# Kernel tuning notes

Hardware: AMD Instinct MI355X
Metric: run time of the kernel (lower is better)

## Reference

```python
import jax, jax.numpy as jnp
import numpy as np

BETA = 0.25
NUM_EMBEDDINGS = 512
DIM_EMBEDDING = 64


def setup_inputs() -> dict:
    key = jax.random.key(0)
    k1, k2 = jax.random.split(key)
    z_e = jax.random.normal(k1, (32, 64, 64, 64), dtype=jnp.float32)
    # torch init: uniform_(-1/num_embeddings, 1/num_embeddings)
    lim = 1.0 / NUM_EMBEDDINGS
    embeddings = jax.random.uniform(
        k2, (NUM_EMBEDDINGS, DIM_EMBEDDING), dtype=jnp.float32,
        minval=-lim, maxval=lim)
    return {"z_e": z_e, "embeddings": embeddings}


def reference(z_e, embeddings):
    # Flatten exactly as torch's z_e.view(-1, dim_embedding) on (N,C,H,W)
    z_flat = z_e.reshape(-1, DIM_EMBEDDING)          # [M, D]
    # Squared euclidean distances: ||z||^2 + ||e||^2 - 2 z e^T
    distances = (
        jnp.sum(z_flat ** 2, axis=1, keepdims=True)
        + jnp.sum(embeddings ** 2, axis=1)
        - 2.0 * jnp.matmul(z_flat, embeddings.T)
    )                                                # [M, K]
    encoding_indices = jnp.argmin(distances, axis=1)[:, None]  # [M, 1]
    quantized = embeddings[encoding_indices[:, 0]].reshape(z_e.shape)
    # Straight-through estimator
    quantized_st = z_e + jax.lax.stop_gradient(quantized - z_e)
    recon_loss = jnp.mean((jax.lax.stop_gradient(quantized_st) - z_e) ** 2)
    commitment_loss = BETA * jnp.mean(
        (quantized_st - jax.lax.stop_gradient(z_e)) ** 2)
    loss = recon_loss + commitment_loss
    return (loss, quantized_st, encoding_indices)
```

## Files before the change

### kernel.cpp

```cpp
#include <hip/hip_runtime.h>
#include <hip/hip_bf16.h>

constexpr int NELEM = 8388608;
constexpr int ROWS  = 64;
constexpr int NBLK  = 131072 / ROWS;
constexpr int ZS    = 68;
constexpr float EPS = 1e-3f;
constexpr int QCAP  = 1024;

typedef short bf16x8 __attribute__((ext_vector_type(8)));
typedef float v4f    __attribute__((ext_vector_type(4)));

__device__ bf16x8 g_efrag[32][2][64];
__device__ float  g_en2[512];

__device__ inline bf16x8 cvt_hi8(const float* __restrict__ s, float scale) {
    bf16x8 h;
#pragma unroll
    for (int j = 0; j < 8; ++j) {
        __hip_bfloat16 b = __float2bfloat16(scale * s[j]);
        h[j] = (short)__bfloat16_as_ushort(b);
    }
    return h;
}

__global__ void __launch_bounds__(256) vq_prep(const float* __restrict__ emb,
                                               float* __restrict__ out) {
    const int b = blockIdx.x;
    if (b < 16) {
        const int id   = b * 256 + threadIdx.x;
        const int lane = id & 63;
        const int kc   = (id >> 6) & 1;
        const int ct   = id >> 7;
        const float* src = emb + (size_t)(ct * 16 + (lane & 15)) * 64
                               + kc * 32 + (lane >> 4) * 8;
        g_efrag[ct][kc][lane] = cvt_hi8(src, -2.0f);
    } else {
#pragma unroll
        for (int c = 0; c < 2; ++c) {
            const int k = threadIdx.x + c * 256;
            const float4* e4 = (const float4*)(emb + (size_t)k * 64);
            float a = 0.f, bq = 0.f, cc = 0.f, d = 0.f;
#pragma unroll
            for (int i = 0; i < 16; ++i) {
                float4 v = e4[i];
                a += v.x * v.x; bq += v.y * v.y; cc += v.z * v.z; d += v.w * v.w;
            }
            g_en2[k] = (a + bq) + (cc + d);
        }
        if (threadIdx.x == 0) out[0] = 0.f;
    }
}

__global__ __launch_bounds__(256) __attribute__((amdgpu_waves_per_eu(4, 4)))
void vq_main(const float* __restrict__ z,
             const float* __restrict__ emb,
             float* __restrict__ out) {
    __shared__ float s_z[ROWS * ZS];
    __shared__ float s_en2[512];
    __shared__ float s_zn2[ROWS];
    __shared__ unsigned long long s_key[ROWS];
    __shared__ unsigned s_q[QCAP];
    __shared__ int s_qn;
    __shared__ float s_lpart[4];

    const int tid  = threadIdx.x;
    const int lane = tid & 63;
    const int wid  = __builtin_amdgcn_readfirstlane(tid >> 6);
    const int mcol = lane & 15;
    const int quad = lane >> 4;

    {
        const int row = tid >> 2, seg = tid & 3;
        const float4* gp = (const float4*)(z + ((size_t)blockIdx.x * ROWS + row) * 64 + seg * 16);
#pragma unroll
        for (int i = 0; i < 4; ++i)
            *(float4*)&s_z[row * ZS + seg * 16 + i * 4] = gp[i];
    }
    s_en2[tid]       = g_en2[tid];
    s_en2[tid + 256] = g_en2[tid + 256];
    if (tid < ROWS) s_key[tid] = ~0ULL;
    if (tid == 0) s_qn = 0;
    __syncthreads();

    {
        const int row = tid >> 2, s = tid & 3;
        const float* zr = &s_z[row * ZS];
        float p = 0.f;
#pragma unroll
        for (int i = 0; i < 16; ++i) p += zr[4 * i + s] * zr[4 * i + s];
        p += __shfl_xor(p, 1, 64);
        p += __shfl_xor(p, 2, 64);
        if (s == 0) s_zn2[row] = p;
    }

    const int zrow = wid * 16 + mcol;
    const bf16x8 zf0 = cvt_hi8(&s_z[zrow * ZS +  0 + quad * 8], 1.0f);
    const bf16x8 zf1 = cvt_hi8(&s_z[zrow * ZS + 32 + quad * 8], 1.0f);

    float lmin = 3.402823466e38f;
#pragma unroll 4
    for (int ct = 0; ct < 32; ++ct) {
        bf16x8 e0 = g_efrag[ct][0][lane];
        bf16x8 e1 = g_efrag[ct][1][lane];
        v4f a = *(const v4f*)&s_en2[ct * 16 + quad * 4];
        a = __builtin_amdgcn_mfma_f32_16x16x32_bf16(e0, zf0, a, 0, 0, 0);
        a = __builtin_amdgcn_mfma_f32_16x16x32_bf16(e1, zf1, a, 0, 0, 0);
        lmin = fminf(lmin, fminf(fminf(a.x, a.y), fminf(a.z, a.w)));
    }
    lmin = fminf(lmin, __shfl_xor(lmin, 16, 64));
    lmin = fminf(lmin, __shfl_xor(lmin, 32, 64));
    const float thr = lmin + EPS;

#pragma unroll 4
    for (int ct = 0; ct < 32; ++ct) {
        bf16x8 e0 = g_efrag[ct][0][lane];
        bf16x8 e1 = g_efrag[ct][1][lane];
        v4f a = *(const v4f*)&s_en2[ct * 16 + quad * 4];
        a = __builtin_amdgcn_mfma_f32_16x16x32_bf16(e0, zf0, a, 0, 0, 0);
        a = __builtin_amdgcn_mfma_f32_16x16x32_bf16(e1, zf1, a, 0, 0, 0);
        float m4 = fminf(fminf(a.x, a.y), fminf(a.z, a.w));
        if (m4 <= thr) {
#pragma unroll
            for (int r = 0; r < 4; ++r) {
                if (a[r] <= thr) {
                    int slot = atomicAdd(&s_qn, 1);
                    if (slot < QCAP)
                        s_q[slot] = ((unsigned)zrow << 16) |
                                    (unsigned)(ct * 16 + quad * 4 + r);
                }
            }
        }
    }
    __syncthreads();

    {
        const int qn = s_qn;
        for (int i = tid; i < qn && i < QCAP; i += 256) {
            const unsigned e = s_q[i];
            const int row = e >> 16, code = e & 0xFFFF;
            const float* zr = &s_z[row * ZS];
            const float* er = emb + (size_t)code * 64;
            float a = 0.f, b = 0.f, c2 = 0.f, d = 0.f;
#pragma unroll
            for (int g = 0; g < 16; ++g) {
                a  += zr[4*g]   * er[4*g];   b += zr[4*g+1] * er[4*g+1];
                c2 += zr[4*g+2] * er[4*g+2]; d += zr[4*g+3] * er[4*g+3];
            }
            float dot  = (a + b) + (c2 + d);
            float dist = (s_zn2[row] + s_en2[code]) - 2.0f * dot;
            unsigned long long key =
                ((unsigned long long)__float_as_uint(dist) << 32) | (unsigned)code;
            atomicMin(&s_key[row], key);
        }
    }
    __syncthreads();

    const int row = tid >> 2, seg = tid & 3;
    const int widx = (int)(unsigned)(s_key[row] & 0x1FFULL);
    const float* er = emb + (size_t)widx * 64 + seg * 16;
    const float* zr = &s_z[row * ZS + seg * 16];
    float* qo = out + 1 + ((size_t)blockIdx.x * ROWS + row) * 64 + seg * 16;
    float lsum = 0.f;
#pragma unroll
    for (int j = 0; j < 16; ++j) {
        float zv = zr[j], ev = er[j];
        float q = zv + (ev - zv);
        float df = q - zv; lsum += df * df;
        qo[j] = q;
    }
    if (seg == 0)
        out[1 + NELEM + blockIdx.x * ROWS + row] = (float)widx;

#pragma unroll
    for (int off = 32; off; off >>= 1) lsum += __shfl_down(lsum, off, 64);
    if (lane == 0) s_lpart[wid] = lsum;
    __syncthreads();
    if (tid == 0) {
        float p = (s_lpart[0] + s_lpart[1]) + (s_lpart[2] + s_lpart[3]);
        atomicAdd(out, p * (1.25f / 8388608.0f));
    }
}

extern "C" void kernel_launch(void* const* d_in, const int* in_sizes, int n_in,
                              void* d_out, int out_size, void* d_ws, size_t ws_size,
                              hipStream_t stream) {
    const float* z   = (const float*)d_in[0];
    const float* emb = (const float*)d_in[1];
    float* out = (float*)d_out;

    vq_prep<<<17, 256, 0, stream>>>(emb, out);
    vq_main<<<NBLK, 256, 0, stream>>>(z, emb, out);
}
```

Baseline: 144.1 us.

## Cache MFMA distances as packed fp16 and make VQ main loop wave-local

The second MFMA pass that recomputed all distances is replaced by storing the scores as packed fp16 in registers during the first pass and scanning them for candidates. Each wave now owns its 16 rows end to end, with per-wave candidate queues, so the block-wide barriers between stages are gone. Each block processes four 64-row tiles in a persistent loop, and the occupancy hint drops to 2 waves per EU. This trades the doubled MFMA and embedding-fragment traffic for heavy register use and lower occupancy. The widened epsilon is meant to cover fp16 rounding, but a larger candidate set could overflow the per-wave queue.

```diff
diff --git a/kernel.cpp b/kernel.cpp
--- a/kernel.cpp
+++ b/kernel.cpp
@@ -3,10 +3,11 @@
 
 constexpr int NELEM = 8388608;
 constexpr int ROWS  = 64;
-constexpr int NBLK  = 131072 / ROWS;
+constexpr int TPB   = 4;
+constexpr int NBLK  = 131072 / ROWS / TPB;
 constexpr int ZS    = 68;
-constexpr float EPS = 1e-3f;
-constexpr int QCAP  = 1024;
+constexpr float EPS = 2e-3f;
+constexpr int QW    = 512;
 
 typedef short bf16x8 __attribute__((ext_vector_type(8)));
 typedef float v4f    __attribute__((ext_vector_type(4)));
@@ -22,6 +23,25 @@
         h[j] = (short)__bfloat16_as_ushort(b);
     }
     return h;
+}
+
+__device__ inline unsigned pkrne2(float a, float b) {
+    union { _Float16 h; unsigned short s; } ca, cb;
+    ca.h = (_Float16)a;
+    cb.h = (_Float16)b;
+    return (unsigned)ca.s | ((unsigned)cb.s << 16);
+}
+__device__ inline unsigned pkmin2(unsigned a, unsigned b) {
+    unsigned d; asm("v_pk_min_f16 %0, %1, %2" : "=v"(d) : "v"(a), "v"(b));
+    return d;
+}
+__device__ inline float h2lo(unsigned u) {
+    union { unsigned short s; _Float16 h; } c; c.s = (unsigned short)(u & 0xffffu);
+    return (float)c.h;
+}
+__device__ inline float h2hi(unsigned u) {
+    union { unsigned short s; _Float16 h; } c; c.s = (unsigned short)(u >> 16);
+    return (float)c.h;
 }
 
 __global__ void __launch_bounds__(256) vq_prep(const float* __restrict__ emb,
@@ -52,7 +72,7 @@
     }
 }
 
-__global__ __launch_bounds__(256) __attribute__((amdgpu_waves_per_eu(4, 4)))
+__global__ __launch_bounds__(256) __attribute__((amdgpu_waves_per_eu(2, 2)))
 void vq_main(const float* __restrict__ z,
              const float* __restrict__ emb,
              float* __restrict__ out) {
@@ -60,8 +80,8 @@
     __shared__ float s_en2[512];
     __shared__ float s_zn2[ROWS];
     __shared__ unsigned long long s_key[ROWS];
-    __shared__ unsigned s_q[QCAP];
-    __shared__ int s_qn;
+    __shared__ unsigned s_qw[4 * QW];
+    __shared__ int s_qnw[4];
     __shared__ float s_lpart[4];
 
     const int tid  = threadIdx.x;
@@ -69,112 +89,137 @@
     const int wid  = __builtin_amdgcn_readfirstlane(tid >> 6);
     const int mcol = lane & 15;
     const int quad = lane >> 4;
-
-    {
-        const int row = tid >> 2, seg = tid & 3;
-        const float4* gp = (const float4*)(z + ((size_t)blockIdx.x * ROWS + row) * 64 + seg * 16);
-#pragma unroll
-        for (int i = 0; i < 4; ++i)
-            *(float4*)&s_z[row * ZS + seg * 16 + i * 4] = gp[i];
-    }
+    const int rl4  = lane >> 2, seg = lane & 3;
+    const int myrow = wid * 16 + rl4;
+    const int zrow  = wid * 16 + mcol;
+
     s_en2[tid]       = g_en2[tid];
     s_en2[tid + 256] = g_en2[tid + 256];
-    if (tid < ROWS) s_key[tid] = ~0ULL;
-    if (tid == 0) s_qn = 0;
+    if (lane < 16) s_key[wid * 16 + lane] = ~0ULL;
+    if (lane == 0) s_qnw[wid] = 0;
     __syncthreads();
 
-    {
-        const int row = tid >> 2, s = tid & 3;
-        const float* zr = &s_z[row * ZS];
-        float p = 0.f;
-#pragma unroll
-        for (int i = 0; i < 16; ++i) p += zr[4 * i + s] * zr[4 * i + s];
-        p += __shfl_xor(p, 1, 64);
-        p += __shfl_xor(p, 2, 64);
-        if (s == 0) s_zn2[row] = p;
-    }
-
-    const int zrow = wid * 16 + mcol;
-    const bf16x8 zf0 = cvt_hi8(&s_z[zrow * ZS +  0 + quad * 8], 1.0f);
-    const bf16x8 zf1 = cvt_hi8(&s_z[zrow * ZS + 32 + quad * 8], 1.0f);
-
-    float lmin = 3.402823466e38f;
-#pragma unroll 4
-    for (int ct = 0; ct < 32; ++ct) {
-        bf16x8 e0 = g_efrag[ct][0][lane];
-        bf16x8 e1 = g_efrag[ct][1][lane];
-        v4f a = *(const v4f*)&s_en2[ct * 16 + quad * 4];
-        a = __builtin_amdgcn_mfma_f32_16x16x32_bf16(e0, zf0, a, 0, 0, 0);
-        a = __builtin_amdgcn_mfma_f32_16x16x32_bf16(e1, zf1, a, 0, 0, 0);
-        lmin = fminf(lmin, fminf(fminf(a.x, a.y), fminf(a.z, a.w)));
-    }
-    lmin = fminf(lmin, __shfl_xor(lmin, 16, 64));
-    lmin = fminf(lmin, __shfl_xor(lmin, 32, 64));
-    const float thr = lmin + EPS;
-
-#pragma unroll 4
-    for (int ct = 0; ct < 32; ++ct) {
-        bf16x8 e0 = g_efrag[ct][0][lane];
-        bf16x8 e1 = g_efrag[ct][1][lane];
-        v4f a = *(const v4f*)&s_en2[ct * 16 + quad * 4];
-        a = __builtin_amdgcn_mfma_f32_16x16x32_bf16(e0, zf0, a, 0, 0, 0);
-        a = __builtin_amdgcn_mfma_f32_16x16x32_bf16(e1, zf1, a, 0, 0, 0);
-        float m4 = fminf(fminf(a.x, a.y), fminf(a.z, a.w));
-        if (m4 <= thr) {
-#pragma unroll
-            for (int r = 0; r < 4; ++r) {
-                if (a[r] <= thr) {
-                    int slot = atomicAdd(&s_qn, 1);
-                    if (slot < QCAP)
-                        s_q[slot] = ((unsigned)zrow << 16) |
-                                    (unsigned)(ct * 16 + quad * 4 + r);
+    float lacc = 0.f;
+
+    for (int t = 0; t < TPB; ++t) {
+        const size_t tb = (size_t)(blockIdx.x * TPB + t) * ROWS;
+
+        {
+            const float4* gp = (const float4*)(z + (tb + myrow) * 64 + seg * 16);
+            float4 v0 = gp[0], v1 = gp[1], v2 = gp[2], v3 = gp[3];
+            float* d = &s_z[myrow * ZS + seg * 16];
+            *(float4*)&d[0] = v0;  *(float4*)&d[4]  = v1;
+            *(float4*)&d[8] = v2;  *(float4*)&d[12] = v3;
+        }
+
+        {
+            const float* zr = &s_z[myrow * ZS];
+            float p = 0.f;
+#pragma unroll
+            for (int i = 0; i < 16; ++i) p += zr[4 * i + seg] * zr[4 * i + seg];
+            p += __shfl_xor(p, 1, 64);
+            p += __shfl_xor(p, 2, 64);
+            if (seg == 0) s_zn2[myrow] = p;
+        }
+
+        const bf16x8 zf0 = cvt_hi8(&s_z[zrow * ZS +  0 + quad * 8], 1.0f);
+        const bf16x8 zf1 = cvt_hi8(&s_z[zrow * ZS + 32 + quad * 8], 1.0f);
+
+        unsigned sc0[16], sc1[16], sc2[16], sc3[16];
+        unsigned mh = 0x7c007c00u;
+
+        auto dense8 = [&](int base, unsigned (&sc)[16]) {
+#pragma unroll
+            for (int c = 0; c < 8; ++c) {
+                const int ct = base + c;
+                bf16x8 e0 = g_efrag[ct][0][lane];
+                bf16x8 e1 = g_efrag[ct][1][lane];
+                v4f a = *(const v4f*)&s_en2[ct * 16 + quad * 4];
+                a = __builtin_amdgcn_mfma_f32_16x16x32_bf16(e0, zf0, a, 0, 0, 0);
+                a = __builtin_amdgcn_mfma_f32_16x16x32_bf16(e1, zf1, a, 0, 0, 0);
+                unsigned p0 = pkrne2(a.x, a.y);
+                unsigned p1 = pkrne2(a.z, a.w);
+                sc[2 * c]     = p0;
+                sc[2 * c + 1] = p1;
+                mh = pkmin2(mh, pkmin2(p0, p1));
+            }
+        };
+        dense8(0,  sc0); __builtin_amdgcn_sched_barrier(0);
+        dense8(8,  sc1); __builtin_amdgcn_sched_barrier(0);
+        dense8(16, sc2); __builtin_amdgcn_sched_barrier(0);
+        dense8(24, sc3);
+
+        float fmn = fminf(h2lo(mh), h2hi(mh));
+        fmn = fminf(fmn, __shfl_xor(fmn, 16, 64));
+        fmn = fminf(fmn, __shfl_xor(fmn, 32, 64));
+        const float thr = fmn + EPS;
+
+        auto push = [&](int code) {
+            int slot = atomicAdd(&s_qnw[wid], 1);
+            if (slot < QW)
+                s_qw[wid * QW + slot] = ((unsigned)zrow << 16) | (unsigned)code;
+        };
+        auto scan8 = [&](int base, const unsigned (&sc)[16]) {
+#pragma unroll
+            for (int c = 0; c < 8; ++c) {
+                unsigned pm = pkmin2(sc[2 * c], sc[2 * c + 1]);
+                if (fminf(h2lo(pm), h2hi(pm)) <= thr) {
+                    const int code0 = (base + c) * 16 + quad * 4;
+                    if (h2lo(sc[2 * c])     <= thr) push(code0 + 0);
+                    if (h2hi(sc[2 * c])     <= thr) push(code0 + 1);
+                    if (h2lo(sc[2 * c + 1]) <= thr) push(code0 + 2);
+                    if (h2hi(sc[2 * c + 1]) <= thr) push(code0 + 3);
                 }
             }
-        }
-    }
-    __syncthreads();
-
-    {
-        const int qn = s_qn;
-        for (int i = tid; i < qn && i < QCAP; i += 256) {
-            const unsigned e = s_q[i];
-            const int row = e >> 16, code = e & 0xFFFF;
-            const float* zr = &s_z[row * ZS];
-            const float* er = emb + (size_t)code * 64;
-            float a = 0.f, b = 0.f, c2 = 0.f, d = 0.f;
-#pragma unroll
-            for (int g = 0; g < 16; ++g) {
-                a  += zr[4*g]   * er[4*g];   b += zr[4*g+1] * er[4*g+1];
-                c2 += zr[4*g+2] * er[4*g+2]; d += zr[4*g+3] * er[4*g+3];
-            }
-            float dot  = (a + b) + (c2 + d);
-            float dist = (s_zn2[row] + s_en2[code]) - 2.0f * dot;
-            unsigned long long key =
-                ((unsigned long long)__float_as_uint(dist) << 32) | (unsigned)code;
-            atomicMin(&s_key[row], key);
-        }
-    }
-    __syncthreads();
-
-    const int row = tid >> 2, seg = tid & 3;
-    const int widx = (int)(unsigned)(s_key[row] & 0x1FFULL);
-    const float* er = emb + (size_t)widx * 64 + seg * 16;
-    const float* zr = &s_z[row * ZS + seg * 16];
-    float* qo = out + 1 + ((size_t)blockIdx.x * ROWS + row) * 64 + seg * 16;
-    float lsum = 0.f;
-#pragma unroll
-    for (int j = 0; j < 16; ++j) {
-        float zv = zr[j], ev = er[j];
-        float q = zv + (ev - zv);
-        float df = q - zv; lsum += df * df;
-        qo[j] = q;
-    }
-    if (seg == 0)
-        out[1 + NELEM + blockIdx.x * ROWS + row] = (float)widx;
-
-#pragma unroll
-    for (int off = 32; off; off >>= 1) lsum += __shfl_down(lsum, off, 64);
-    if (lane == 0) s_lpart[wid] = lsum;
+        };
+        scan8(0, sc0); scan8(8, sc1); scan8(16, sc2); scan8(24, sc3);
+
+        {
+            const int qn = s_qnw[wid];
+            for (int i = lane; i < qn && i < QW; i += 64) {
+                const unsigned e = s_qw[wid * QW + i];
+                const int row = e >> 16, code = e & 0xFFFF;
+                const float* zr = &s_z[row * ZS];
+                const float* er = emb + (size_t)code * 64;
+                float a = 0.f, b = 0.f, c2 = 0.f, d = 0.f;
+#pragma unroll
+                for (int g = 0; g < 16; ++g) {
+                    a  += zr[4*g]   * er[4*g];   b += zr[4*g+1] * er[4*g+1];
+                    c2 += zr[4*g+2] * er[4*g+2]; d += zr[4*g+3] * er[4*g+3];
+                }
+                float dot  = (a + b) + (c2 + d);
+                float dist = (s_zn2[row] + s_en2[code]) - 2.0f * dot;
+                unsigned long long key =
+                    ((unsigned long long)__float_as_uint(dist) << 32) | (unsigned)code;
+                atomicMin(&s_key[row], key);
+            }
+        }
+
+        {
+            const int widx = (int)(unsigned)(s_key[myrow] & 0x1FFULL);
+            const float* er = emb + (size_t)widx * 64 + seg * 16;
+            const float* zr = &s_z[myrow * ZS + seg * 16];
+            float* qo = out + 1 + (tb + myrow) * 64 + seg * 16;
+            float lsum = 0.f;
+#pragma unroll
+            for (int j = 0; j < 16; ++j) {
+                float zv = zr[j], ev = er[j];
+                float q = zv + (ev - zv);
+                float df = q - zv; lsum += df * df;
+                qo[j] = q;
+            }
+            if (seg == 0)
+                out[1 + NELEM + tb + myrow] = (float)widx;
+#pragma unroll
+            for (int off = 32; off; off >>= 1) lsum += __shfl_down(lsum, off, 64);
+            if (lane == 0) lacc += lsum;
+        }
+
+        if (lane < 16) s_key[wid * 16 + lane] = ~0ULL;
+        if (lane == 0) s_qnw[wid] = 0;
+    }
+
+    if (lane == 0) s_lpart[wid] = lacc;
     __syncthreads();
     if (tid == 0) {
         float p = (s_lpart[0] + s_lpart[1]) + (s_lpart[2] + s_lpart[3]);
```

Result: slower. 215.1 us (+49.2%).
